# Performance work log

Hardware: AMD Instinct MI355X
Metric: run time of the kernel (lower is better)

Reference implementation:

```python
import jax, jax.numpy as jnp
import numpy as np

TAU = 0.05
LAMBDA0 = 1.0
DELTA = 1.0
MU = 0.4

B, D, C = 128, 1024, 32768


def setup_inputs() -> dict:
    key = jax.random.key(0)
    k1, k2, k3 = jax.random.split(key, 3)
    inputs = jax.random.normal(k1, (B, D), jnp.float32)
    inputs = inputs / jnp.linalg.norm(inputs, axis=1, keepdims=True)  # L2-normed features
    em = jax.random.normal(k2, (C, D), jnp.float32)
    em = em / jnp.linalg.norm(em, axis=1, keepdims=True)  # memory bank rows are unit-norm
    targets = jax.random.randint(k3, (B,), 0, C, dtype=jnp.int32)
    return {"inputs": inputs, "em": em, "targets": targets, "epoch": 10}


def _adaptive_selection(scores, targets):
    # scores are detached in the original (inputs.detach().clone())
    s = jax.lax.stop_gradient(scores)
    onehot = (s > LAMBDA0 / TAU).astype(jnp.float32)      # [B, C]
    ks1 = onehot.sum(axis=1)                              # raw neighbor counts (returned)
    mask = (ks1 > 1).astype(jnp.float32)
    k = ks1 * mask + (1.0 - mask) * 2.0
    k = DELTA / (k * jnp.log(k))
    k = (k * mask)[:, None]                               # [B, 1]
    t = onehot * k
    t = t.at[jnp.arange(t.shape[0]), targets].set(1.0)    # scatter 1 at ground-truth class
    return t, ks1


def reference(inputs, em, targets, epoch):
    mu = min(MU / 60.0 * (epoch + 1), 1.0)
    scores = (inputs @ em.T) / TAU                        # [B, C]

    # epoch > 4 path: target_loss with adaptive selection
    targets_line, ks = _adaptive_selection(scores, targets)
    logp = jax.nn.log_softmax(scores, axis=1)
    loss = (-(targets_line * logp).sum(axis=1)).mean()

    # sequential per-sample EMA scatter update with renorm (original does this in backward)
    def step(mem, xy):
        x, y = xy
        row = mu * mem[y] + (1.0 - mu) * x
        row = row / jnp.linalg.norm(row)
        return mem.at[y].set(row), None

    new_em, _ = jax.lax.scan(step, em, (inputs, targets))
    return loss, ks, new_em
```

## Files before the change

kernel.cpp:

```cpp
#include <hip/hip_runtime.h>
#include <math.h>

#define BN 128
#define DN 1024
#define CN 32768
#define NB 64
#define KS 32
#define NBLK (CN / NB)
#define LDA 40

typedef float f32x4 __attribute__((ext_vector_type(4)));
typedef short short8 __attribute__((ext_vector_type(8)));

static __device__ inline unsigned short f2b(float f) {
    union { float f; unsigned u; } v; v.f = f;
    unsigned r = v.u + 0x7FFF + ((v.u >> 16) & 1);
    return (unsigned short)(r >> 16);
}

__global__ __launch_bounds__(256)
void k1_gemm_stats(const float* __restrict__ inp, const float* __restrict__ em,
                   float* __restrict__ out_loss, float* __restrict__ out_em,
                   float* __restrict__ ws)
{
    __shared__ unsigned short Ab[2][BN * LDA];
    __shared__ unsigned short Bb[2][NB * LDA];
    __shared__ float4 smp[BN][4];

    const int t   = threadIdx.x;
    const int blk = blockIdx.x;
    const size_t c0 = (size_t)blk * NB;
    if (blk == 0 && t == 0) out_loss[0] = 0.0f;

    const int w  = t >> 6;
    const int l  = t & 63;
    const int lr = l & 15, lq = l >> 4;

    f32x4 acc[8];
#pragma unroll
    for (int m = 0; m < 8; ++m) acc[m] = (f32x4)0.0f;

    const int arow[4] = { (0*256 + t) >> 3, (1*256 + t) >> 3, (2*256 + t) >> 3, (3*256 + t) >> 3 };
    const int ak4     = t & 7;
    const int bcol[2] = { (0*256 + t) >> 3, (1*256 + t) >> 3 };

    float4 ga0[4], gb0[2], ga1[4], gb1[2];

#define LOADG(kt, GA, GB)                                                         \
    {                                                                             \
        _Pragma("unroll")                                                         \
        for (int p = 0; p < 4; ++p)                                               \
            GA[p] = *(const float4*)&inp[(size_t)arow[p] * DN + (kt) + ak4 * 4];  \
        _Pragma("unroll")                                                         \
        for (int p = 0; p < 2; ++p)                                               \
            GB[p] = *(const float4*)&em[(c0 + bcol[p]) * DN + (kt) + ak4 * 4];    \
    }

#define STAGE(buf, kt, GA, GB)                                                    \
    {                                                                             \
        _Pragma("unroll")                                                         \
        for (int p = 0; p < 4; ++p) {                                             \
            uint2 u;                                                              \
            u.x = (unsigned)f2b(GA[p].x) | ((unsigned)f2b(GA[p].y) << 16);        \
            u.y = (unsigned)f2b(GA[p].z) | ((unsigned)f2b(GA[p].w) << 16);        \
            *(uint2*)&Ab[buf][arow[p] * LDA + ak4 * 4] = u;                       \
        }                                                                         \
        _Pragma("unroll")                                                         \
        for (int p = 0; p < 2; ++p) {                                             \
            uint2 u;                                                              \
            u.x = (unsigned)f2b(GB[p].x) | ((unsigned)f2b(GB[p].y) << 16);        \
            u.y = (unsigned)f2b(GB[p].z) | ((unsigned)f2b(GB[p].w) << 16);        \
            *(uint2*)&Bb[buf][bcol[p] * LDA + ak4 * 4] = u;                       \
            *(float4*)&out_em[(c0 + bcol[p]) * DN + (kt) + ak4 * 4] = GB[p];      \
        }                                                                         \
    }

#define COMPUTE(buf)                                                              \
    {                                                                             \
        const short8 bf = *(const short8*)&Bb[buf][(w * 16 + lr) * LDA + lq * 8]; \
        _Pragma("unroll")                                                         \
        for (int m = 0; m < 8; ++m) {                                             \
            const short8 af = *(const short8*)&Ab[buf][(m * 16 + lr) * LDA + lq * 8]; \
            acc[m] = __builtin_amdgcn_mfma_f32_16x16x32_bf16(af, bf, acc[m], 0, 0, 0); \
        }                                                                         \
    }

    LOADG(0, ga0, gb0)
    for (int kt = 0; kt < DN; kt += 2 * KS) {
        STAGE(0, kt, ga0, gb0)
        __syncthreads();
        LOADG(kt + KS, ga1, gb1)
        COMPUTE(0)

        STAGE(1, kt + KS, ga1, gb1)
        __syncthreads();
        if (kt + 2 * KS < DN) LOADG(kt + 2 * KS, ga0, gb0)
        COMPUTE(1)
    }
    __syncthreads();

#pragma unroll
    for (int m = 0; m < 8; ++m) {
#pragma unroll
        for (int r = 0; r < 4; ++r) {
            float s = acc[m][r] * 20.0f;
            float mx = s;
#pragma unroll
            for (int off = 1; off < 16; off <<= 1) mx = fmaxf(mx, __shfl_xor(mx, off));
            float z   = __expf(s - mx);
            float cnt = (s > 20.0f) ? 1.0f : 0.0f;
            float ss  = (s > 20.0f) ? s : 0.0f;
#pragma unroll
            for (int off = 1; off < 16; off <<= 1) {
                z   += __shfl_xor(z, off);
                cnt += __shfl_xor(cnt, off);
                ss  += __shfl_xor(ss, off);
            }
            if (lr == 0) smp[m * 16 + lq * 4 + r][w] = make_float4(mx, z, cnt, ss);
        }
    }
    __syncthreads();

    if (t < BN) {
        float4 p0 = smp[t][0];
        float M = p0.x, Z = p0.y, CNT = p0.z, SS = p0.w;
#pragma unroll
        for (int q = 1; q < 4; ++q) {
            float4 p = smp[t][q];
            float Mn = fmaxf(M, p.x);
            Z = Z * __expf(M - Mn) + p.y * __expf(p.x - Mn);
            M = Mn; CNT += p.z; SS += p.w;
        }
        ((float4*)ws)[(size_t)t * NBLK + blk] = make_float4(M, Z, CNT, SS);
    }
}

__global__ __launch_bounds__(256)
void k2_finalize(const float* __restrict__ inp, const float* __restrict__ em,
                 const int* __restrict__ tgt, const float* __restrict__ ws,
                 float* __restrict__ d_loss, float* __restrict__ d_ks)
{
    const int i = blockIdx.x;
    const int t = threadIdx.x;
    const int wid = t >> 6, lane = t & 63;
    __shared__ float red[4][4];
    __shared__ float dred[4];

    float m = -INFINITY, z = 0.f, cnt = 0.f, ss = 0.f;
    for (int c = t; c < NBLK; c += 256) {
        float4 wv = ((const float4*)ws)[(size_t)i * NBLK + c];
        float M = fmaxf(m, wv.x);
        z = z * __expf(m - M) + wv.y * __expf(wv.x - M);
        m = M; cnt += wv.z; ss += wv.w;
    }
#pragma unroll
    for (int off = 1; off < 64; off <<= 1) {
        float m2 = __shfl_xor(m, off), z2 = __shfl_xor(z, off);
        float M = fmaxf(m, m2);
        z = z * __expf(m - M) + z2 * __expf(m2 - M);
        m = M;
        cnt += __shfl_xor(cnt, off);
        ss  += __shfl_xor(ss, off);
    }
    if (lane == 0) { red[wid][0] = m; red[wid][1] = z; red[wid][2] = cnt; red[wid][3] = ss; }

    const int y = tgt[i];
    float4 a = *(const float4*)&inp[(size_t)i * DN + t * 4];
    float4 b = *(const float4*)&em[(size_t)y * DN + t * 4];
    float d = a.x * b.x + a.y * b.y + a.z * b.z + a.w * b.w;
#pragma unroll
    for (int off = 1; off < 64; off <<= 1) d += __shfl_xor(d, off);
    if (lane == 0) dred[wid] = d;
    __syncthreads();

    if (t == 0) {
        float M = red[0][0], Z = red[0][1], CNT = red[0][2], SS = red[0][3];
#pragma unroll
        for (int q = 1; q < 4; ++q) {
            float m2 = red[q][0], z2 = red[q][1];
            float Mn = fmaxf(M, m2);
            Z = Z * __expf(M - Mn) + z2 * __expf(m2 - Mn);
            M = Mn; CNT += red[q][2]; SS += red[q][3];
        }
        float sy  = (dred[0] + dred[1] + dred[2] + dred[3]) * 20.0f;
        float lse = M + logf(Z);
        float A   = SS - CNT * lse;
        float ki  = (CNT > 1.0f) ? (1.0f / (CNT * logf(CNT))) : 0.0f;
        float sum_t = ki * (A - ((sy > 20.0f) ? (sy - lse) : 0.0f)) + (sy - lse);
        atomicAdd(d_loss, -sum_t * (1.0f / 128.0f));
        d_ks[i] = CNT;
    }
}

__global__ __launch_bounds__(256)
void k3_ema(const float* __restrict__ inp, const int* __restrict__ tgt,
            const void* __restrict__ epoch_p, float* __restrict__ out_em)
{
    const int j = blockIdx.x;
    const int y = tgt[j];
    for (int p = 0; p < j; ++p)
        if (tgt[p] == y) return;

    int ei = *(const int*)epoch_p;
    float e = (ei >= 0 && ei < 1000000) ? (float)ei : *(const float*)epoch_p;
    const float mu = fminf(0.4f / 60.0f * (e + 1.0f), 1.0f);
    const float om = 1.0f - mu;

    const int t = threadIdx.x;
    const int wid = t >> 6, lane = t & 63;
    __shared__ float nred[4];

    float4 r = *(const float4*)&out_em[(size_t)y * DN + t * 4];
    for (int p = j; p < BN; ++p) {
        if (tgt[p] != y) continue;
        float4 x = *(const float4*)&inp[(size_t)p * DN + t * 4];
        r.x = mu * r.x + om * x.x;
        r.y = mu * r.y + om * x.y;
        r.z = mu * r.z + om * x.z;
        r.w = mu * r.w + om * x.w;
        float n = r.x * r.x + r.y * r.y + r.z * r.z + r.w * r.w;
#pragma unroll
        for (int off = 1; off < 64; off <<= 1) n += __shfl_xor(n, off);
        if (lane == 0) nred[wid] = n;
        __syncthreads();
        n = nred[0] + nred[1] + nred[2] + nred[3];
        float inv = 1.0f / sqrtf(n);
        r.x *= inv; r.y *= inv; r.z *= inv; r.w *= inv;
        __syncthreads();
    }
    *(float4*)&out_em[(size_t)y * DN + t * 4] = r;
}

extern "C" void kernel_launch(void* const* d_in, const int* in_sizes, int n_in,
                              void* d_out, int out_size, void* d_ws, size_t ws_size,
                              hipStream_t stream)
{
    const float* inp = (const float*)d_in[0];
    const float* em  = (const float*)d_in[1];
    const int*   tgt = (const int*)d_in[2];
    const void*  ep  = d_in[3];

    float* loss   = (float*)d_out;
    float* ks     = loss + 1;
    float* out_em = ks + BN;
    float* ws     = (float*)d_ws;

    k1_gemm_stats<<<NBLK, 256, 0, stream>>>(inp, em, loss, out_em, ws);
    k2_finalize<<<BN, 256, 0, stream>>>(inp, em, tgt, ws, loss, ks);
    k3_ema<<<BN, 256, 0, stream>>>(inp, tgt, ep, out_em);
}
```

Baseline: 343.5 us.

## Pre-convert inputs to bf16, drop LDS staging in GEMM, merge finalize and EMA kernels

A new pre-kernel converts the 128x1024 input matrix to bf16 once in workspace, so the GEMM blocks no longer convert it redundantly. The GEMM now reads the bf16 A fragments and fp32 em rows straight from global memory into MFMA registers, removing the shared-memory double buffer and its barriers. The finalize and EMA kernels are merged into one launch, with the EMA reading the original em instead of the copied output. The risk is higher global and L2 traffic, since each block re-reads the shared A matrix directly, and the em loads lose coalescing.

```diff
diff --git a/kernel.cpp b/kernel.cpp
--- a/kernel.cpp
+++ b/kernel.cpp
@@ -5,9 +5,7 @@
 #define DN 1024
 #define CN 32768
 #define NB 64
-#define KS 32
 #define NBLK (CN / NB)
-#define LDA 40
 
 typedef float f32x4 __attribute__((ext_vector_type(4)));
 typedef short short8 __attribute__((ext_vector_type(8)));
@@ -19,85 +17,57 @@
 }
 
 __global__ __launch_bounds__(256)
-void k1_gemm_stats(const float* __restrict__ inp, const float* __restrict__ em,
-                   float* __restrict__ out_loss, float* __restrict__ out_em,
-                   float* __restrict__ ws)
-{
-    __shared__ unsigned short Ab[2][BN * LDA];
-    __shared__ unsigned short Bb[2][NB * LDA];
+void k0_cvt(const float* __restrict__ inp, unsigned short* __restrict__ Abf,
+            float* __restrict__ out_loss)
+{
+    const int i = blockIdx.x * 256 + threadIdx.x;
+    if (i == 0) out_loss[0] = 0.0f;
+    float4 a = *(const float4*)&inp[(size_t)i * 8];
+    float4 b = *(const float4*)&inp[(size_t)i * 8 + 4];
+    short8 s;
+    s[0] = f2b(a.x); s[1] = f2b(a.y); s[2] = f2b(a.z); s[3] = f2b(a.w);
+    s[4] = f2b(b.x); s[5] = f2b(b.y); s[6] = f2b(b.z); s[7] = f2b(b.w);
+    *(short8*)&Abf[(size_t)i * 8] = s;
+}
+
+__global__ __launch_bounds__(256)
+void k1_gemm_stats(const float* __restrict__ em,
+                   const unsigned short* __restrict__ Abf,
+                   float* __restrict__ out_em, float* __restrict__ ws)
+{
     __shared__ float4 smp[BN][4];
 
     const int t   = threadIdx.x;
     const int blk = blockIdx.x;
-    const size_t c0 = (size_t)blk * NB;
-    if (blk == 0 && t == 0) out_loss[0] = 0.0f;
-
-    const int w  = t >> 6;
-    const int l  = t & 63;
-    const int lr = l & 15, lq = l >> 4;
+    const int w   = t >> 6;
+    const int l   = t & 63;
+    const int lr  = l & 15, lq = l >> 4;
+
+    const size_t col = (size_t)blk * NB + w * 16 + lr;
+    const float4* __restrict__ emp  = (const float4*)&em[col * DN];
+    float4* __restrict__       outp = (float4*)&out_em[col * DN];
 
     f32x4 acc[8];
 #pragma unroll
     for (int m = 0; m < 8; ++m) acc[m] = (f32x4)0.0f;
 
-    const int arow[4] = { (0*256 + t) >> 3, (1*256 + t) >> 3, (2*256 + t) >> 3, (3*256 + t) >> 3 };
-    const int ak4     = t & 7;
-    const int bcol[2] = { (0*256 + t) >> 3, (1*256 + t) >> 3 };
-
-    float4 ga0[4], gb0[2], ga1[4], gb1[2];
-
-#define LOADG(kt, GA, GB)                                                         \
-    {                                                                             \
-        _Pragma("unroll")                                                         \
-        for (int p = 0; p < 4; ++p)                                               \
-            GA[p] = *(const float4*)&inp[(size_t)arow[p] * DN + (kt) + ak4 * 4];  \
-        _Pragma("unroll")                                                         \
-        for (int p = 0; p < 2; ++p)                                               \
-            GB[p] = *(const float4*)&em[(c0 + bcol[p]) * DN + (kt) + ak4 * 4];    \
-    }
-
-#define STAGE(buf, kt, GA, GB)                                                    \
-    {                                                                             \
-        _Pragma("unroll")                                                         \
-        for (int p = 0; p < 4; ++p) {                                             \
-            uint2 u;                                                              \
-            u.x = (unsigned)f2b(GA[p].x) | ((unsigned)f2b(GA[p].y) << 16);        \
-            u.y = (unsigned)f2b(GA[p].z) | ((unsigned)f2b(GA[p].w) << 16);        \
-            *(uint2*)&Ab[buf][arow[p] * LDA + ak4 * 4] = u;                       \
-        }                                                                         \
-        _Pragma("unroll")                                                         \
-        for (int p = 0; p < 2; ++p) {                                             \
-            uint2 u;                                                              \
-            u.x = (unsigned)f2b(GB[p].x) | ((unsigned)f2b(GB[p].y) << 16);        \
-            u.y = (unsigned)f2b(GB[p].z) | ((unsigned)f2b(GB[p].w) << 16);        \
-            *(uint2*)&Bb[buf][bcol[p] * LDA + ak4 * 4] = u;                       \
-            *(float4*)&out_em[(c0 + bcol[p]) * DN + (kt) + ak4 * 4] = GB[p];      \
-        }                                                                         \
-    }
-
-#define COMPUTE(buf)                                                              \
-    {                                                                             \
-        const short8 bf = *(const short8*)&Bb[buf][(w * 16 + lr) * LDA + lq * 8]; \
-        _Pragma("unroll")                                                         \
-        for (int m = 0; m < 8; ++m) {                                             \
-            const short8 af = *(const short8*)&Ab[buf][(m * 16 + lr) * LDA + lq * 8]; \
-            acc[m] = __builtin_amdgcn_mfma_f32_16x16x32_bf16(af, bf, acc[m], 0, 0, 0); \
-        }                                                                         \
-    }
-
-    LOADG(0, ga0, gb0)
-    for (int kt = 0; kt < DN; kt += 2 * KS) {
-        STAGE(0, kt, ga0, gb0)
-        __syncthreads();
-        LOADG(kt + KS, ga1, gb1)
-        COMPUTE(0)
-
-        STAGE(1, kt + KS, ga1, gb1)
-        __syncthreads();
-        if (kt + 2 * KS < DN) LOADG(kt + 2 * KS, ga0, gb0)
-        COMPUTE(1)
-    }
-    __syncthreads();
+#pragma unroll 2
+    for (int kt = 0; kt < DN; kt += 32) {
+        const int kv = (kt >> 2) + lq * 2;
+        const float4 b0 = emp[kv];
+        const float4 b1 = emp[kv + 1];
+        outp[kv]     = b0;
+        outp[kv + 1] = b1;
+        short8 bf;
+        bf[0] = f2b(b0.x); bf[1] = f2b(b0.y); bf[2] = f2b(b0.z); bf[3] = f2b(b0.w);
+        bf[4] = f2b(b1.x); bf[5] = f2b(b1.y); bf[6] = f2b(b1.z); bf[7] = f2b(b1.w);
+        const int ko = kt + lq * 8;
+#pragma unroll
+        for (int m = 0; m < 8; ++m) {
+            const short8 af = *(const short8*)&Abf[(size_t)(m * 16 + lr) * DN + ko];
+            acc[m] = __builtin_amdgcn_mfma_f32_16x16x32_bf16(af, bf, acc[m], 0, 0, 0);
+        }
+    }
 
 #pragma unroll
     for (int m = 0; m < 8; ++m) {
@@ -136,67 +106,70 @@
 }
 
 __global__ __launch_bounds__(256)
-void k2_finalize(const float* __restrict__ inp, const float* __restrict__ em,
-                 const int* __restrict__ tgt, const float* __restrict__ ws,
-                 float* __restrict__ d_loss, float* __restrict__ d_ks)
-{
-    const int i = blockIdx.x;
-    const int t = threadIdx.x;
-    const int wid = t >> 6, lane = t & 63;
+void k23(const float* __restrict__ inp, const float* __restrict__ em,
+         const int* __restrict__ tgt, const float* __restrict__ ws,
+         const void* __restrict__ epoch_p,
+         float* __restrict__ d_loss, float* __restrict__ d_ks,
+         float* __restrict__ out_em)
+{
     __shared__ float red[4][4];
     __shared__ float dred[4];
-
-    float m = -INFINITY, z = 0.f, cnt = 0.f, ss = 0.f;
-    for (int c = t; c < NBLK; c += 256) {
-        float4 wv = ((const float4*)ws)[(size_t)i * NBLK + c];
-        float M = fmaxf(m, wv.x);
-        z = z * __expf(m - M) + wv.y * __expf(wv.x - M);
-        m = M; cnt += wv.z; ss += wv.w;
-    }
-#pragma unroll
-    for (int off = 1; off < 64; off <<= 1) {
-        float m2 = __shfl_xor(m, off), z2 = __shfl_xor(z, off);
-        float M = fmaxf(m, m2);
-        z = z * __expf(m - M) + z2 * __expf(m2 - M);
-        m = M;
-        cnt += __shfl_xor(cnt, off);
-        ss  += __shfl_xor(ss, off);
-    }
-    if (lane == 0) { red[wid][0] = m; red[wid][1] = z; red[wid][2] = cnt; red[wid][3] = ss; }
-
-    const int y = tgt[i];
-    float4 a = *(const float4*)&inp[(size_t)i * DN + t * 4];
-    float4 b = *(const float4*)&em[(size_t)y * DN + t * 4];
-    float d = a.x * b.x + a.y * b.y + a.z * b.z + a.w * b.w;
-#pragma unroll
-    for (int off = 1; off < 64; off <<= 1) d += __shfl_xor(d, off);
-    if (lane == 0) dred[wid] = d;
-    __syncthreads();
-
-    if (t == 0) {
-        float M = red[0][0], Z = red[0][1], CNT = red[0][2], SS = red[0][3];
-#pragma unroll
-        for (int q = 1; q < 4; ++q) {
-            float m2 = red[q][0], z2 = red[q][1];
-            float Mn = fmaxf(M, m2);
-            Z = Z * __expf(M - Mn) + z2 * __expf(m2 - Mn);
-            M = Mn; CNT += red[q][2]; SS += red[q][3];
-        }
-        float sy  = (dred[0] + dred[1] + dred[2] + dred[3]) * 20.0f;
-        float lse = M + logf(Z);
-        float A   = SS - CNT * lse;
-        float ki  = (CNT > 1.0f) ? (1.0f / (CNT * logf(CNT))) : 0.0f;
-        float sum_t = ki * (A - ((sy > 20.0f) ? (sy - lse) : 0.0f)) + (sy - lse);
-        atomicAdd(d_loss, -sum_t * (1.0f / 128.0f));
-        d_ks[i] = CNT;
-    }
-}
-
-__global__ __launch_bounds__(256)
-void k3_ema(const float* __restrict__ inp, const int* __restrict__ tgt,
-            const void* __restrict__ epoch_p, float* __restrict__ out_em)
-{
-    const int j = blockIdx.x;
+    __shared__ float nred[4];
+
+    const int bid = blockIdx.x;
+    const int t   = threadIdx.x;
+    const int wid = t >> 6, lane = t & 63;
+
+    if (bid < BN) {
+        const int i = bid;
+        float m = -INFINITY, z = 0.f, cnt = 0.f, ss = 0.f;
+        for (int c = t; c < NBLK; c += 256) {
+            float4 wv = ((const float4*)ws)[(size_t)i * NBLK + c];
+            float M = fmaxf(m, wv.x);
+            z = z * __expf(m - M) + wv.y * __expf(wv.x - M);
+            m = M; cnt += wv.z; ss += wv.w;
+        }
+#pragma unroll
+        for (int off = 1; off < 64; off <<= 1) {
+            float m2 = __shfl_xor(m, off), z2 = __shfl_xor(z, off);
+            float M = fmaxf(m, m2);
+            z = z * __expf(m - M) + z2 * __expf(m2 - M);
+            m = M;
+            cnt += __shfl_xor(cnt, off);
+            ss  += __shfl_xor(ss, off);
+        }
+        if (lane == 0) { red[wid][0] = m; red[wid][1] = z; red[wid][2] = cnt; red[wid][3] = ss; }
+
+        const int y = tgt[i];
+        float4 a = *(const float4*)&inp[(size_t)i * DN + t * 4];
+        float4 b = *(const float4*)&em[(size_t)y * DN + t * 4];
+        float d = a.x * b.x + a.y * b.y + a.z * b.z + a.w * b.w;
+#pragma unroll
+        for (int off = 1; off < 64; off <<= 1) d += __shfl_xor(d, off);
+        if (lane == 0) dred[wid] = d;
+        __syncthreads();
+
+        if (t == 0) {
+            float M = red[0][0], Z = red[0][1], CNT = red[0][2], SS = red[0][3];
+#pragma unroll
+            for (int q = 1; q < 4; ++q) {
+                float m2 = red[q][0], z2 = red[q][1];
+                float Mn = fmaxf(M, m2);
+                Z = Z * __expf(M - Mn) + z2 * __expf(m2 - Mn);
+                M = Mn; CNT += red[q][2]; SS += red[q][3];
+            }
+            float sy  = (dred[0] + dred[1] + dred[2] + dred[3]) * 20.0f;
+            float lse = M + logf(Z);
+            float A   = SS - CNT * lse;
+            float ki  = (CNT > 1.0f) ? (1.0f / (CNT * logf(CNT))) : 0.0f;
+            float sum_t = ki * (A - ((sy > 20.0f) ? (sy - lse) : 0.0f)) + (sy - lse);
+            atomicAdd(d_loss, -sum_t * (1.0f / 128.0f));
+            d_ks[i] = CNT;
+        }
+        return;
+    }
+
+    const int j = bid - BN;
     const int y = tgt[j];
     for (int p = 0; p < j; ++p)
         if (tgt[p] == y) return;
@@ -206,11 +179,7 @@
     const float mu = fminf(0.4f / 60.0f * (e + 1.0f), 1.0f);
     const float om = 1.0f - mu;
 
-    const int t = threadIdx.x;
-    const int wid = t >> 6, lane = t & 63;
-    __shared__ float nred[4];
-
-    float4 r = *(const float4*)&out_em[(size_t)y * DN + t * 4];
+    float4 r = *(const float4*)&em[(size_t)y * DN + t * 4];
     for (int p = j; p < BN; ++p) {
         if (tgt[p] != y) continue;
         float4 x = *(const float4*)&inp[(size_t)p * DN + t * 4];
@@ -243,9 +212,11 @@
     float* loss   = (float*)d_out;
     float* ks     = loss + 1;
     float* out_em = ks + BN;
-    float* ws     = (float*)d_ws;
-
-    k1_gemm_stats<<<NBLK, 256, 0, stream>>>(inp, em, loss, out_em, ws);
-    k2_finalize<<<BN, 256, 0, stream>>>(inp, em, tgt, ws, loss, ks);
-    k3_ema<<<BN, 256, 0, stream>>>(inp, tgt, ep, out_em);
-}
+
+    float* ws = (float*)d_ws;
+    unsigned short* Abf = (unsigned short*)(ws + (size_t)BN * NBLK * 4);
+
+    k0_cvt<<<BN * DN / (256 * 8), 256, 0, stream>>>(inp, Abf, loss);
+    k1_gemm_stats<<<NBLK, 256, 0, stream>>>(em, Abf, out_em, ws);
+    k23<<<2 * BN, 256, 0, stream>>>(inp, em, tgt, ws, ep, loss, ks, out_em);
+}
```

New measurement: 355.6 us. 3.5% more time.
